# Optimization experiments

Hardware: AMD Instinct MI355X
Metric: run time of the kernel (lower is better)

The kernel has to match this reference:

```python
import jax, jax.numpy as jnp
import numpy as np

B, S, D_IN, H, L = 8, 4096, 256, 512, 2
EPS = 1e-5


def layer_norm(x, w, b):
    mu = x.mean(axis=-1, keepdims=True)
    var = ((x - mu) ** 2).mean(axis=-1, keepdims=True)
    return (x - mu) * jax.lax.rsqrt(var + EPS) * w + b


def rwkv_scan(k, v):
    # wkv_t = sigmoid(k_t)*v_t + alpha_{t-1};  alpha_t = sigmoid(k_t)*v_t + 0.9*alpha_{t-1}
    s = jax.nn.sigmoid(k) * v  # [B,S,H]
    def step(alpha, s_t):
        wkv_t = s_t + alpha
        return s_t + 0.9 * alpha, wkv_t
    _, wkv = jax.lax.scan(step, jnp.zeros_like(s[:, 0]), jnp.swapaxes(s, 0, 1))
    return jnp.swapaxes(wkv, 0, 1)


def setup_inputs() -> dict:
    key = jax.random.key(0)
    ks = jax.random.split(key, 16)
    sc = 1.0 / np.sqrt(H)
    return {
        "x": jax.random.normal(ks[0], (B, S, D_IN), jnp.float32),
        "W_in": jax.random.normal(ks[1], (H, D_IN), jnp.float32) / np.sqrt(D_IN),
        "b_in": jnp.zeros((H,), jnp.float32),
        "tm_k": jax.random.normal(ks[2], (L, H), jnp.float32),
        "tm_v": jax.random.normal(ks[3], (L, H), jnp.float32),
        "tm_r": jax.random.normal(ks[4], (L, H), jnp.float32),
        "Wk": jax.random.normal(ks[5], (L, H, H), jnp.float32) * sc,
        "Wv": jax.random.normal(ks[6], (L, H, H), jnp.float32) * sc,
        "Wr": jax.random.normal(ks[7], (L, H, H), jnp.float32) * sc,
        "Wo": jax.random.normal(ks[8], (L, H, H), jnp.float32) * sc,
        "ln1_w": jnp.ones((L, H), jnp.float32),
        "ln1_b": jnp.zeros((L, H), jnp.float32),
        "ln2_w": jnp.ones((L, H), jnp.float32),
        "ln2_b": jnp.zeros((L, H), jnp.float32),
    }


def reference(x, W_in, b_in, tm_k, tm_v, tm_r, Wk, Wv, Wr, Wo, ln1_w, ln1_b, ln2_w, ln2_b):
    h = jnp.einsum('bsd,hd->bsh', x, W_in) + b_in  # input projection
    for l in range(L):
        mean = h.mean(axis=1, keepdims=True)  # [B,1,H]
        xk = h * tm_k[l] + (1 - tm_k[l]) * mean
        xv = h * tm_v[l] + (1 - tm_v[l]) * mean
        xr = h * tm_r[l] + (1 - tm_r[l]) * mean
        k = jax.nn.relu(jnp.einsum('bsh,oh->bso', xk, Wk[l]))
        v = jax.nn.relu(jnp.einsum('bsh,oh->bso', xv, Wv[l]))
        r = jax.nn.sigmoid(jnp.einsum('bsh,oh->bso', xr, Wr[l]))
        wkv = rwkv_scan(k, v)
        out = jnp.einsum('bsh,oh->bso', r * wkv, Wo[l])
        out = layer_norm(h + out, ln1_w[l], ln1_b[l])
        ff = jax.nn.relu(layer_norm(out, ln2_w[l], ln2_b[l]))
        h = out + ff
    return h
```

## Files before the change

kernel.cpp:

```cpp
#include <hip/hip_runtime.h>
#include <hip/hip_bf16.h>
#include <cstdint>
#include <cstddef>

#define S_LEN 4096
#define HDIM  512
#define BDIM  8
#define DIN   256
#define NLAYER 2

using float4v = __attribute__((ext_vector_type(4))) float;
using short8  = __attribute__((ext_vector_type(8))) short;
using bf16x8  = __attribute__((ext_vector_type(8))) __bf16;

struct __align__(8) us4_t { unsigned short x, y, z, w; };

__device__ __forceinline__ unsigned short f2bf(float f) {
    return __builtin_bit_cast(unsigned short, (__bf16)f);
}
__device__ __forceinline__ float bf2f(unsigned short s) {
    union { unsigned u; float f; } v; v.u = ((unsigned)s) << 16;
    return v.f;
}
__device__ __forceinline__ float fast_rcp(float x) { return __builtin_amdgcn_rcpf(x); }
__device__ __forceinline__ float fast_rsq(float x) { return __builtin_amdgcn_rsqf(x); }

__device__ __forceinline__ float4v mfma_bf16(short8 a, short8 b, float4v c) {
    return __builtin_amdgcn_mfma_f32_16x16x32_bf16(
        __builtin_bit_cast(bf16x8, a), __builtin_bit_cast(bf16x8, b), c, 0, 0, 0);
}
__device__ __forceinline__ float wave_sum(float v) {
#pragma unroll
    for (int m = 1; m < 64; m <<= 1) v += __shfl_xor(v, m, 64);
    return v;
}
__device__ __forceinline__ void gload16(const void* g, void* l) {
    __builtin_amdgcn_global_load_lds(
        (const __attribute__((address_space(1))) unsigned int*)g,
        (__attribute__((address_space(3))) unsigned int*)l,
        16, 0, 0);
}

#define VMW_ASM(N) asm volatile("s_waitcnt vmcnt(" #N ")" ::: "memory")
template<int N> __device__ __forceinline__ void vmwait() {
    static_assert(N == 0 || N == 4 || N == 5 || N == 6 || N == 8 || N == 10,
                  "add a case for this N");
    if constexpr (N == 0) VMW_ASM(0);
    else if constexpr (N == 4) VMW_ASM(4);
    else if constexpr (N == 5) VMW_ASM(5);
    else if constexpr (N == 6) VMW_ASM(6);
    else if constexpr (N == 8) VMW_ASM(8);
    else if constexpr (N == 10) VMW_ASM(10);
}
#define LGKM0()    asm volatile("s_waitcnt lgkmcnt(0)" ::: "memory")
#define RBARRIER() asm volatile("s_barrier" ::: "memory")

__global__ void cvt4_k(const float* __restrict__ a, unsigned short* __restrict__ oa, int na4,
                       const float* __restrict__ b, unsigned short* __restrict__ ob, int nb4,
                       const float* __restrict__ c, unsigned short* __restrict__ oc2, int nc4,
                       const float* __restrict__ Wk, const float* __restrict__ Wv,
                       const float* __restrict__ Wr,
                       const float* __restrict__ tmk, const float* __restrict__ tmv,
                       const float* __restrict__ tmr,
                       unsigned short* __restrict__ Wf, int nf4)
{
    int i = blockIdx.x * blockDim.x + threadIdx.x;
    if (i < na4 + nb4 + nc4) {
        const float* src; unsigned short* dst; int idx;
        if (i < na4)            { src = a; dst = oa;  idx = i; }
        else if (i < na4 + nb4) { src = b; dst = ob;  idx = i - na4; }
        else                    { src = c; dst = oc2; idx = i - na4 - nb4; }
        float4 v = ((const float4*)src)[idx];
        us4_t o;
        o.x = f2bf(v.x); o.y = f2bf(v.y); o.z = f2bf(v.z); o.w = f2bf(v.w);
        ((us4_t*)dst)[idx] = o;
        return;
    }
    int fi = i - (na4 + nb4 + nc4);
    if (fi >= nf4) return;
    int e = fi * 4;
    const int HH = HDIM * HDIM;
    int l   = (e >= 3 * HH) ? 1 : 0;
    int rem = e - l * 3 * HH;
    int j   = rem >> 18;
    int ok  = rem & (HH - 1);
    int k   = ok & (HDIM - 1);
    const float* W = (j == 0) ? Wk : (j == 1) ? Wv : Wr;
    const float* t = (j == 0) ? tmk : (j == 1) ? tmv : tmr;
    float4 w = *(const float4*)(W + (size_t)l * HH + ok);
    const float* tp = t + l * HDIM + k;
    us4_t o;
    o.x = f2bf(w.x * tp[0]); o.y = f2bf(w.y * tp[1]);
    o.z = f2bf(w.z * tp[2]); o.w = f2bf(w.w * tp[3]);
    *(us4_t*)(Wf + e) = o;
}

__global__ void meanbias_k(const float* __restrict__ msum_l, float invS,
    const float* __restrict__ Wk, const float* __restrict__ Wv, const float* __restrict__ Wr,
    const float* __restrict__ tmk, const float* __restrict__ tmv, const float* __restrict__ tmr,
    float* __restrict__ mb)
{
    __shared__ float m2[HDIM];
    const int j = blockIdx.x, b = blockIdx.y, oc = blockIdx.z;
    const int tid = threadIdx.x, lane = tid & 63, wid = tid >> 6;
    const float* W = (j == 0) ? Wk : (j == 1) ? Wv : Wr;
    const float* t = (j == 0) ? tmk : (j == 1) ? tmv : tmr;
    for (int i = tid; i < HDIM; i += 256)
        m2[i] = msum_l[b * HDIM + i] * invS * (1.f - t[i]);
    __syncthreads();
    const int o0 = oc * 64 + wid * 16;
    for (int oo = 0; oo < 16; oo++) {
        int o = o0 + oo;
        const float* wr_ = W + (size_t)o * HDIM + lane * 8;
        float4 w0 = *(const float4*)wr_;
        float4 w1 = *(const float4*)(wr_ + 4);
        const float* mp = m2 + lane * 8;
        float s = w0.x * mp[0] + w0.y * mp[1] + w0.z * mp[2] + w0.w * mp[3]
                + w1.x * mp[4] + w1.y * mp[5] + w1.z * mp[6] + w1.w * mp[7];
        s = wave_sum(s);
        if (lane == 0) mb[((size_t)j * BDIM + b) * HDIM + o] = s;
    }
}

template<int TM, int BN, int NMAT, int EPI, int K, int NY, int NW>
__global__ __launch_bounds__(NW * 64, 2) void gemm2_k(
    const unsigned short* __restrict__ A,
    const unsigned short* __restrict__ B0,
    const unsigned short* __restrict__ B1,
    const unsigned short* __restrict__ B2,
    const float* __restrict__ mb,
    unsigned short* __restrict__ outB0,
    unsigned short* __restrict__ outB1,
    float* __restrict__ msum_out)
{
    constexpr int NTHR = NW * 64;
    constexpr int NT   = K / 64;
    static_assert(NT >= 2, "pipeline needs >=2 K-tiles");
    constexpr int ROWS = TM + NMAT * BN;
    constexpr int NC   = ROWS / 8;
    static_assert(NC % NW == 0, "chunks must split evenly across waves");
    constexpr int NCW  = NC / NW;
    constexpr int WC   = NW / 2;
    constexpr int MI   = TM / 32;
    constexpr int CW   = BN / WC;
    constexpr int NI   = CW / 16;
    static_assert(NI >= 1, "");
    __shared__ __align__(16) unsigned short smem[2][ROWS * 64];
    static_assert((EPI == 1 ? 2 : 1) * TM * (BN + 8) <= 2 * ROWS * 64,
                  "epilogue overflow");

    const int tid = threadIdx.x, lane = tid & 63, wid = tid >> 6;
    const int wr = wid / WC, wc = wid % WC;
    const int chunk = gridDim.x >> 3;
    const int logical = (blockIdx.x & 7) * chunk + (blockIdx.x >> 3);
    const int m0 = (logical / NY) * TM, n0 = (logical % NY) * BN;

    const int l8 = lane >> 3;
    const int soff = (((lane & 7) ^ l8) * 16);
    const char* gp[NCW];
#pragma unroll
    for (int i = 0; i < NCW; i++) {
        int c = wid * NCW + i;
        const unsigned short* base; int row;
        if (c < TM / 8) { base = A; row = m0 + c * 8 + l8; }
        else {
            int cb = c - TM / 8;
            int j  = cb / (BN / 8);
            int rl = (cb % (BN / 8)) * 8 + l8;
            base = (j == 0) ? B0 : ((j == 1) ? B1 : B2);
            row  = n0 + rl;
        }
        gp[i] = (const char*)base + (size_t)row * (K * 2) + soff;
    }

    float4v acc[NMAT][MI][NI];
#pragma unroll
    for (int j = 0; j < NMAT; j++)
#pragma unroll
        for (int mi = 0; mi < MI; mi++)
#pragma unroll
            for (int ni = 0; ni < NI; ni++)
                acc[j][mi][ni] = (float4v){0.f, 0.f, 0.f, 0.f};

    auto STAGE = [&](int buf) {
#pragma unroll
        for (int i = 0; i < NCW; i++) {
            gload16(gp[i], (char*)&smem[buf][0] + (unsigned)(wid * NCW + i) * 1024);
            gp[i] += 128;
        }
    };

    STAGE(0);
    STAGE(1);
    for (int t = 0; t < NT; t++) {
        if (t == NT - 1) vmwait<0>(); else vmwait<NCW>();
        RBARRIER();
        const int cur = t & 1;
        const unsigned short* As = &smem[cur][0];
        const unsigned short* Bs = &smem[cur][TM * 64];
#pragma unroll
        for (int kk = 0; kk < 2; kk++) {
            short8 a_[MI];
#pragma unroll
            for (int mi = 0; mi < MI; mi++) {
                int row = wr * (TM / 2) + mi * 16 + (lane & 15);
                int sl  = (kk * 4 + (lane >> 4)) ^ (row & 7);
                a_[mi] = *(const short8*)&As[row * 64 + sl * 8];
            }
#pragma unroll
            for (int ni = 0; ni < NI; ni++) {
                int rowb = wc * CW + ni * 16 + (lane & 15);
                int slb  = (kk * 4 + (lane >> 4)) ^ (rowb & 7);
#pragma unroll
                for (int j = 0; j < NMAT; j++) {
                    short8 b_ = *(const short8*)&Bs[(j * BN + rowb) * 64 + slb * 8];
#pragma unroll
                    for (int mi = 0; mi < MI; mi++)
                        acc[j][mi][ni] = mfma_bf16(a_[mi], b_, acc[j][mi][ni]);
                }
            }
        }
        LGKM0();
        RBARRIER();
        if (t + 2 < NT) STAGE(cur);
    }

    const int bidx  = m0 >> 12;
    const int rbl   = wr * (TM / 2) + (lane >> 4) * 4;
    const int cbl   = wc * CW + (lane & 15);

    if constexpr (EPI == 0) {
        constexpr int BNP = BN + 8;
        unsigned short* tile = &smem[0][0];
        float csum[NI];
#pragma unroll
        for (int ni = 0; ni < NI; ni++) csum[ni] = 0.f;
#pragma unroll
        for (int ni = 0; ni < NI; ni++) {
            float bb = mb[n0 + cbl + ni * 16];
#pragma unroll
            for (int mi = 0; mi < MI; mi++) {
#pragma unroll
                for (int r = 0; r < 4; r++) {
                    float val = acc[0][mi][ni][r] + bb;
                    tile[(rbl + mi * 16 + r) * BNP + cbl + ni * 16] = f2bf(val);
                    csum[ni] += val;
                }
            }
        }
        __syncthreads();
        constexpr int QR = BN / 8;
        for (int idx = tid; idx < TM * QR; idx += NTHR) {
            int row = idx / QR, q = idx % QR;
            int4 v = *(const int4*)&tile[row * BNP + q * 8];
            *(int4*)(outB0 + (size_t)(m0 + row) * HDIM + n0 + q * 8) = v;
        }
#pragma unroll
        for (int ni = 0; ni < NI; ni++) {
            float sc = csum[ni];
            sc += __shfl_xor(sc, 16, 64);
            sc += __shfl_xor(sc, 32, 64);
            if (lane < 16)
                atomicAdd(&msum_out[bidx * HDIM + n0 + wc * CW + ni * 16 + lane], sc);
        }
    } else if constexpr (EPI == 1) {
        constexpr int BNP = BN + 8;
        unsigned short* tS = &smem[0][0];
        unsigned short* tR = &smem[0][0] + TM * BNP;
#pragma unroll
        for (int ni = 0; ni < NI; ni++) {
            int gcol = n0 + cbl + ni * 16;
            float mk = mb[(0 * BDIM + bidx) * HDIM + gcol];
            float mv = mb[(1 * BDIM + bidx) * HDIM + gcol];
            float mr = mb[(2 * BDIM + bidx) * HDIM + gcol];
#pragma unroll
            for (int mi = 0; mi < MI; mi++) {
#pragma unroll
                for (int r = 0; r < 4; r++) {
                    float kk_ = fmaxf(acc[0][mi][ni][r] + mk, 0.f);
                    float vv  = fmaxf(acc[NMAT > 1 ? 1 : 0][mi][ni][r] + mv, 0.f);
                    float rr  = fast_rcp(1.f + __expf(-(acc[NMAT > 2 ? 2 : 0][mi][ni][r] + mr)));
                    float sv  = vv * fast_rcp(1.f + __expf(-kk_));
                    int loc = (rbl + mi * 16 + r) * BNP + cbl + ni * 16;
                    tS[loc] = f2bf(sv);
                    tR[loc] = f2bf(rr);
                }
            }
        }
        __syncthreads();
        constexpr int QR = BN / 8;
        for (int idx = tid; idx < 2 * TM * QR; idx += NTHR) {
            int tn = idx / (TM * QR), rem = idx % (TM * QR);
            int row = rem / QR, q = rem % QR;
            int4 v = *(const int4*)&smem[0][tn * TM * BNP + row * BNP + q * 8];
            unsigned short* dst = tn ? outB1 : outB0;
            *(int4*)(dst + (size_t)(m0 + row) * HDIM + n0 + q * 8) = v;
        }
    } else {
        constexpr int BNP = BN + 8;
        unsigned short* tile = &smem[0][0];
#pragma unroll
        for (int ni = 0; ni < NI; ni++) {
#pragma unroll
            for (int mi = 0; mi < MI; mi++) {
#pragma unroll
                for (int r = 0; r < 4; r++)
                    tile[(rbl + mi * 16 + r) * BNP + cbl + ni * 16] = f2bf(acc[0][mi][ni][r]);
            }
        }
        __syncthreads();
        constexpr int QR = BN / 8;
        for (int idx = tid; idx < TM * QR; idx += NTHR) {
            int row = idx / QR, q = idx % QR;
            int4 v = *(const int4*)&tile[row * BNP + q * 8];
            *(int4*)(outB0 + (size_t)(m0 + row) * HDIM + n0 + q * 8) = v;
        }
    }
}

__global__ void scan_k(const unsigned short* __restrict__ s_bf,
                       const unsigned short* __restrict__ r_bf,
                       unsigned short* __restrict__ y_bf)
{
    const int C = 64, W = 64;
    const int b  = blockIdx.z;
    const int t0 = blockIdx.x * C;
    const int h2 = threadIdx.x * 2;
    const size_t rowbase = (size_t)b * S_LEN;

    float a0 = 0.f, a1 = 0.f;
    int tstart = t0 - W; if (tstart < 0) tstart = 0;
#pragma unroll 4
    for (int t = tstart; t < t0; t++) {
        unsigned u = *(const unsigned*)(s_bf + (rowbase + t) * HDIM + h2);
        a0 = bf2f((unsigned short)(u & 0xffff)) + 0.9f * a0;
        a1 = bf2f((unsigned short)(u >> 16))    + 0.9f * a1;
    }
#pragma unroll 4
    for (int t = t0; t < t0 + C; t++) {
        size_t off = (rowbase + t) * HDIM + h2;
        unsigned u  = *(const unsigned*)(s_bf + off);
        unsigned ur = *(const unsigned*)(r_bf + off);
        float s0 = bf2f((unsigned short)(u & 0xffff));
        float s1 = bf2f((unsigned short)(u >> 16));
        float w0 = s0 + a0, w1v = s1 + a1;
        a0 = s0 + 0.9f * a0;
        a1 = s1 + 0.9f * a1;
        float r0 = bf2f((unsigned short)(ur & 0xffff));
        float r1 = bf2f((unsigned short)(ur >> 16));
        unsigned outp = (unsigned)f2bf(r0 * w0) | ((unsigned)f2bf(r1 * w1v) << 16);
        *(unsigned*)(y_bf + off) = outp;
    }
}

__global__ __launch_bounds__(256) void lnfuse_k(
    const unsigned short* __restrict__ Hb, const unsigned short* __restrict__ O,
    const float* __restrict__ w1, const float* __restrict__ b1,
    const float* __restrict__ w2, const float* __restrict__ b2,
    float* __restrict__ dstF, unsigned short* __restrict__ dst_bf,
    float* __restrict__ msum_next)
{
    __shared__ float red[HDIM];
    const int b    = blockIdx.y;
    const int tid  = threadIdx.x;
    const int wid  = tid >> 6, lane = tid & 63;
    const int wglob = blockIdx.x * 4 + wid;
    const int c0   = lane * 8;

    float w1v[8], b1v[8], w2v[8], b2v[8];
#pragma unroll
    for (int j = 0; j < 8; j++) {
        w1v[j] = w1[c0 + j]; b1v[j] = b1[c0 + j];
        w2v[j] = w2[c0 + j]; b2v[j] = b2[c0 + j];
    }
    float macc[8] = {0.f, 0.f, 0.f, 0.f, 0.f, 0.f, 0.f, 0.f};

    for (int s = wglob; s < S_LEN; s += 512) {
        size_t ro = ((size_t)b * S_LEN + s) * HDIM + c0;
        int4 hv4 = *(const int4*)(Hb + ro);
        int4 ov4 = *(const int4*)(O + ro);
        const unsigned short* hu = (const unsigned short*)&hv4;
        const unsigned short* ou = (const unsigned short*)&ov4;
        float x[8];
#pragma unroll
        for (int j = 0; j < 8; j++) x[j] = bf2f(hu[j]) + bf2f(ou[j]);
        float sm = 0.f;
#pragma unroll
        for (int j = 0; j < 8; j++) sm += x[j];
        float mu = wave_sum(sm) * (1.f / HDIM);
        float sq = 0.f;
#pragma unroll
        for (int j = 0; j < 8; j++) { float d = x[j] - mu; sq += d * d; }
        float rs = fast_rsq(wave_sum(sq) * (1.f / HDIM) + 1e-5f);
        float out[8];
#pragma unroll
        for (int j = 0; j < 8; j++) out[j] = (x[j] - mu) * rs * w1v[j] + b1v[j];
        float sm2 = 0.f;
#pragma unroll
        for (int j = 0; j < 8; j++) sm2 += out[j];
        float mu2 = wave_sum(sm2) * (1.f / HDIM);
        float sq2 = 0.f;
#pragma unroll
        for (int j = 0; j < 8; j++) { float d = out[j] - mu2; sq2 += d * d; }
        float rs2 = fast_rsq(wave_sum(sq2) * (1.f / HDIM) + 1e-5f);
        float hn[8];
#pragma unroll
        for (int j = 0; j < 8; j++) {
            float ff = fmaxf(0.f, (out[j] - mu2) * rs2 * w2v[j] + b2v[j]);
            hn[j] = out[j] + ff;
            macc[j] += hn[j];
        }
        if (dstF) {
            float4 o1 = {hn[0], hn[1], hn[2], hn[3]};
            float4 o2 = {hn[4], hn[5], hn[6], hn[7]};
            *(float4*)(dstF + ro) = o1;
            *(float4*)(dstF + ro + 4) = o2;
        }
        if (dst_bf) {
            unsigned q[4];
#pragma unroll
            for (int j = 0; j < 4; j++)
                q[j] = (unsigned)f2bf(hn[2 * j]) | ((unsigned)f2bf(hn[2 * j + 1]) << 16);
            *(int4*)(dst_bf + ro) = *(int4*)q;
        }
    }

    if (msum_next) {
        for (int i = tid; i < HDIM; i += 256) red[i] = 0.f;
        __syncthreads();
#pragma unroll
        for (int j = 0; j < 8; j++) atomicAdd(&red[c0 + j], macc[j]);
        __syncthreads();
        for (int i = tid; i < HDIM; i += 256)
            atomicAdd(&msum_next[b * HDIM + i], red[i]);
    }
}

extern "C" void kernel_launch(void* const* d_in, const int* in_sizes, int n_in,
                              void* d_out, int out_size, void* d_ws, size_t ws_size,
                              hipStream_t stream)
{
    const float* x   = (const float*)d_in[0];
    const float* Win = (const float*)d_in[1];
    const float* bin = (const float*)d_in[2];
    const float* tmk = (const float*)d_in[3];
    const float* tmv = (const float*)d_in[4];
    const float* tmr = (const float*)d_in[5];
    const float* Wk  = (const float*)d_in[6];
    const float* Wv  = (const float*)d_in[7];
    const float* Wr  = (const float*)d_in[8];
    const float* Wo  = (const float*)d_in[9];
    const float* l1w = (const float*)d_in[10];
    const float* l1b = (const float*)d_in[11];
    const float* l2w = (const float*)d_in[12];
    const float* l2b = (const float*)d_in[13];

    char* ws = (char*)d_ws;
    size_t off = 0;
    auto alloc = [&](size_t bytes) -> char* {
        char* p = ws + off;
        off += (bytes + 255) & ~(size_t)255;
        return p;
    };
    const size_t NTOK = (size_t)BDIM * S_LEN;
    const size_t HH = (size_t)HDIM * HDIM;
    unsigned short* region0 = (unsigned short*)alloc(NTOK * HDIM * 2);
    unsigned short* x_bf   = region0;
    unsigned short* y_bf   = region0;
    unsigned short* Win_bf = (unsigned short*)alloc((size_t)HDIM * DIN * 2);
    unsigned short* Wo_bf  = (unsigned short*)alloc(NLAYER * HH * 2);
    unsigned short* Wf     = (unsigned short*)alloc(NLAYER * 3 * HH * 2);
    unsigned short* h_bf   = (unsigned short*)alloc(NTOK * HDIM * 2);
    unsigned short* h2_bf  = (unsigned short*)alloc(NTOK * HDIM * 2);
    unsigned short* s_bf   = (unsigned short*)alloc(NTOK * HDIM * 2);
    unsigned short* r_bf   = (unsigned short*)alloc(NTOK * HDIM * 2);
    unsigned short* o_bf   = (unsigned short*)alloc(NTOK * HDIM * 2);
    float*          msum   = (float*)alloc(2 * BDIM * HDIM * 4);
    float*          mbuf   = (float*)alloc(3 * BDIM * HDIM * 4);

    hipMemsetAsync(msum, 0, 2 * BDIM * HDIM * 4, stream);

    {
        int na4 = (int)(NTOK * DIN / 4);
        int nb4 = (int)((size_t)HDIM * DIN / 4);
        int nc4 = (int)(NLAYER * HH / 4);
        int nf4 = (int)(NLAYER * 3 * HH / 4);
        int tot = na4 + nb4 + nc4 + nf4;
        cvt4_k<<<(tot + 255) / 256, 256, 0, stream>>>(
            x, x_bf, na4, Win, Win_bf, nb4, Wo, Wo_bf, nc4,
            Wk, Wv, Wr, tmk, tmv, tmr, Wf, nf4);
    }

    const float invS = 1.f / S_LEN;

    gemm2_k<128, 128, 1, 0, DIN, 4, 4><<<1024, 256, 0, stream>>>(
        x_bf, Win_bf, nullptr, nullptr, bin, h_bf, nullptr, msum);

    for (int l = 0; l < NLAYER; l++) {
        const unsigned short* hl = (l == 0) ? h_bf : h2_bf;
        meanbias_k<<<dim3(3, BDIM, 8), 256, 0, stream>>>(
            msum + (size_t)l * BDIM * HDIM, invS,
            Wk + (size_t)l * HH, Wv + (size_t)l * HH, Wr + (size_t)l * HH,
            tmk + l * HDIM, tmv + l * HDIM, tmr + l * HDIM, mbuf);
        gemm2_k<128, 64, 3, 1, HDIM, 8, 8><<<2048, 512, 0, stream>>>(
            hl,
            Wf + ((size_t)l * 3 + 0) * HH, Wf + ((size_t)l * 3 + 1) * HH,
            Wf + ((size_t)l * 3 + 2) * HH,
            mbuf, s_bf, r_bf, nullptr);
        scan_k<<<dim3(S_LEN / 64, 1, BDIM), 256, 0, stream>>>(s_bf, r_bf, y_bf);
        gemm2_k<128, 128, 1, 3, HDIM, 4, 4><<<1024, 256, 0, stream>>>(
            y_bf, Wo_bf + (size_t)l * HH, nullptr, nullptr,
            nullptr, o_bf, nullptr, nullptr);
        lnfuse_k<<<dim3(128, BDIM), 256, 0, stream>>>(
            hl, o_bf, l1w + l * HDIM, l1b + l * HDIM, l2w + l * HDIM, l2b + l * HDIM,
            (l == 0) ? nullptr : (float*)d_out,
            (l == 0) ? h2_bf : nullptr,
            (l == 0) ? (msum + BDIM * HDIM) : nullptr);
    }
}
```

Baseline: 316.2 us.

## Fuse output projection GEMM with residual double layernorm epilogue

Replaces the separate Wo GEMM plus lnfuse kernel with one GEMM that uses full-row tiles (TM=64, BN=512), so each block owns complete rows and can run residual add, both layernorms, ReLU and the mean-sum accumulation in its epilogue. This removes the o_bf intermediate write and re-read and one kernel launch. In exchange the GEMM grid shrinks to 512 blocks with larger tiles, which may lower occupancy and change how well the tiling performs.

```diff
diff --git a/kernel.cpp b/kernel.cpp
--- a/kernel.cpp
+++ b/kernel.cpp
@@ -43,13 +43,14 @@
 
 #define VMW_ASM(N) asm volatile("s_waitcnt vmcnt(" #N ")" ::: "memory")
 template<int N> __device__ __forceinline__ void vmwait() {
-    static_assert(N == 0 || N == 4 || N == 5 || N == 6 || N == 8 || N == 10,
+    static_assert(N == 0 || N == 4 || N == 5 || N == 6 || N == 8 || N == 9 || N == 10,
                   "add a case for this N");
     if constexpr (N == 0) VMW_ASM(0);
     else if constexpr (N == 4) VMW_ASM(4);
     else if constexpr (N == 5) VMW_ASM(5);
     else if constexpr (N == 6) VMW_ASM(6);
     else if constexpr (N == 8) VMW_ASM(8);
+    else if constexpr (N == 9) VMW_ASM(9);
     else if constexpr (N == 10) VMW_ASM(10);
 }
 #define LGKM0()    asm volatile("s_waitcnt lgkmcnt(0)" ::: "memory")
@@ -129,8 +130,12 @@
     const unsigned short* __restrict__ B1,
     const unsigned short* __restrict__ B2,
     const float* __restrict__ mb,
+    const float* __restrict__ mb2,
+    const float* __restrict__ mb3,
+    const float* __restrict__ mb4,
     unsigned short* __restrict__ outB0,
     unsigned short* __restrict__ outB1,
+    float* __restrict__ dstF,
     float* __restrict__ msum_out)
 {
     constexpr int NTHR = NW * 64;
@@ -146,7 +151,8 @@
     constexpr int NI   = CW / 16;
     static_assert(NI >= 1, "");
     __shared__ __align__(16) unsigned short smem[2][ROWS * 64];
-    static_assert((EPI == 1 ? 2 : 1) * TM * (BN + 8) <= 2 * ROWS * 64,
+    static_assert((EPI == 4 ? TM * (BN + 12) * 2
+                            : (EPI == 1 ? 2 : 1) * TM * (BN + 8)) <= 2 * ROWS * 64,
                   "epilogue overflow");
 
     const int tid = threadIdx.x, lane = tid & 63, wid = tid >> 6;
@@ -295,6 +301,92 @@
             int4 v = *(const int4*)&smem[0][tn * TM * BNP + row * BNP + q * 8];
             unsigned short* dst = tn ? outB1 : outB0;
             *(int4*)(dst + (size_t)(m0 + row) * HDIM + n0 + q * 8) = v;
+        }
+    } else if constexpr (EPI == 4) {
+        constexpr int BNP4 = BN + 12;
+        float* ftile = (float*)&smem[0][0];
+#pragma unroll
+        for (int ni = 0; ni < NI; ni++)
+#pragma unroll
+            for (int mi = 0; mi < MI; mi++)
+#pragma unroll
+                for (int r = 0; r < 4; r++)
+                    ftile[(rbl + mi * 16 + r) * BNP4 + cbl + ni * 16] = acc[0][mi][ni][r];
+        __syncthreads();
+        const int c0 = lane * 8;
+        float w1v[8], b1v[8], w2v[8], b2v[8];
+#pragma unroll
+        for (int j = 0; j < 8; j++) {
+            w1v[j] = mb[c0 + j];  b1v[j] = mb2[c0 + j];
+            w2v[j] = mb3[c0 + j]; b2v[j] = mb4[c0 + j];
+        }
+        constexpr int RPW = TM / NW;
+        float macc[8] = {0.f, 0.f, 0.f, 0.f, 0.f, 0.f, 0.f, 0.f};
+        int4 hv[RPW];
+#pragma unroll
+        for (int rr = 0; rr < RPW; rr++) {
+            int row = wid * RPW + rr;
+            hv[rr] = *(const int4*)(B1 + (size_t)(m0 + row) * HDIM + c0);
+        }
+#pragma unroll
+        for (int rr = 0; rr < RPW; rr++) {
+            int row = wid * RPW + rr;
+            const unsigned short* hu = (const unsigned short*)&hv[rr];
+            const float* op = &ftile[row * BNP4 + c0];
+            float x[8];
+#pragma unroll
+            for (int j = 0; j < 8; j++) x[j] = bf2f(hu[j]) + op[j];
+            float sm = 0.f;
+#pragma unroll
+            for (int j = 0; j < 8; j++) sm += x[j];
+            float mu = wave_sum(sm) * (1.f / HDIM);
+            float sq = 0.f;
+#pragma unroll
+            for (int j = 0; j < 8; j++) { float d = x[j] - mu; sq += d * d; }
+            float rs = fast_rsq(wave_sum(sq) * (1.f / HDIM) + 1e-5f);
+            float out[8];
+#pragma unroll
+            for (int j = 0; j < 8; j++) out[j] = (x[j] - mu) * rs * w1v[j] + b1v[j];
+            float sm2 = 0.f;
+#pragma unroll
+            for (int j = 0; j < 8; j++) sm2 += out[j];
+            float mu2 = wave_sum(sm2) * (1.f / HDIM);
+            float sq2 = 0.f;
+#pragma unroll
+            for (int j = 0; j < 8; j++) { float d = out[j] - mu2; sq2 += d * d; }
+            float rs2 = fast_rsq(wave_sum(sq2) * (1.f / HDIM) + 1e-5f);
+            float hn[8];
+#pragma unroll
+            for (int j = 0; j < 8; j++) {
+                float ff = fmaxf(0.f, (out[j] - mu2) * rs2 * w2v[j] + b2v[j]);
+                hn[j] = out[j] + ff;
+                macc[j] += hn[j];
+            }
+            size_t ro = (size_t)(m0 + row) * HDIM + c0;
+            if (dstF) {
+                float4 o1 = {hn[0], hn[1], hn[2], hn[3]};
+                float4 o2 = {hn[4], hn[5], hn[6], hn[7]};
+                *(float4*)(dstF + ro) = o1;
+                *(float4*)(dstF + ro + 4) = o2;
+            }
+            if (outB0) {
+                unsigned q[4];
+#pragma unroll
+                for (int j = 0; j < 4; j++)
+                    q[j] = (unsigned)f2bf(hn[2 * j]) | ((unsigned)f2bf(hn[2 * j + 1]) << 16);
+                *(int4*)(outB0 + ro) = *(int4*)q;
+            }
+        }
+        if (msum_out) {
+            __syncthreads();
+            float* red = ftile;
+            if (tid < HDIM) red[tid] = 0.f;
+            __syncthreads();
+#pragma unroll
+            for (int j = 0; j < 8; j++) atomicAdd(&red[c0 + j], macc[j]);
+            __syncthreads();
+            if (tid < HDIM)
+                atomicAdd(&msum_out[bidx * HDIM + tid], red[tid]);
         }
     } else {
         constexpr int BNP = BN + 8;
@@ -350,89 +442,6 @@
         float r1 = bf2f((unsigned short)(ur >> 16));
         unsigned outp = (unsigned)f2bf(r0 * w0) | ((unsigned)f2bf(r1 * w1v) << 16);
         *(unsigned*)(y_bf + off) = outp;
-    }
-}
-
-__global__ __launch_bounds__(256) void lnfuse_k(
-    const unsigned short* __restrict__ Hb, const unsigned short* __restrict__ O,
-    const float* __restrict__ w1, const float* __restrict__ b1,
-    const float* __restrict__ w2, const float* __restrict__ b2,
-    float* __restrict__ dstF, unsigned short* __restrict__ dst_bf,
-    float* __restrict__ msum_next)
-{
-    __shared__ float red[HDIM];
-    const int b    = blockIdx.y;
-    const int tid  = threadIdx.x;
-    const int wid  = tid >> 6, lane = tid & 63;
-    const int wglob = blockIdx.x * 4 + wid;
-    const int c0   = lane * 8;
-
-    float w1v[8], b1v[8], w2v[8], b2v[8];
-#pragma unroll
-    for (int j = 0; j < 8; j++) {
-        w1v[j] = w1[c0 + j]; b1v[j] = b1[c0 + j];
-        w2v[j] = w2[c0 + j]; b2v[j] = b2[c0 + j];
-    }
-    float macc[8] = {0.f, 0.f, 0.f, 0.f, 0.f, 0.f, 0.f, 0.f};
-
-    for (int s = wglob; s < S_LEN; s += 512) {
-        size_t ro = ((size_t)b * S_LEN + s) * HDIM + c0;
-        int4 hv4 = *(const int4*)(Hb + ro);
-        int4 ov4 = *(const int4*)(O + ro);
-        const unsigned short* hu = (const unsigned short*)&hv4;
-        const unsigned short* ou = (const unsigned short*)&ov4;
-        float x[8];
-#pragma unroll
-        for (int j = 0; j < 8; j++) x[j] = bf2f(hu[j]) + bf2f(ou[j]);
-        float sm = 0.f;
-#pragma unroll
-        for (int j = 0; j < 8; j++) sm += x[j];
-        float mu = wave_sum(sm) * (1.f / HDIM);
-        float sq = 0.f;
-#pragma unroll
-        for (int j = 0; j < 8; j++) { float d = x[j] - mu; sq += d * d; }
-        float rs = fast_rsq(wave_sum(sq) * (1.f / HDIM) + 1e-5f);
-        float out[8];
-#pragma unroll
-        for (int j = 0; j < 8; j++) out[j] = (x[j] - mu) * rs * w1v[j] + b1v[j];
-        float sm2 = 0.f;
-#pragma unroll
-        for (int j = 0; j < 8; j++) sm2 += out[j];
-        float mu2 = wave_sum(sm2) * (1.f / HDIM);
-        float sq2 = 0.f;
-#pragma unroll
-        for (int j = 0; j < 8; j++) { float d = out[j] - mu2; sq2 += d * d; }
-        float rs2 = fast_rsq(wave_sum(sq2) * (1.f / HDIM) + 1e-5f);
-        float hn[8];
-#pragma unroll
-        for (int j = 0; j < 8; j++) {
-            float ff = fmaxf(0.f, (out[j] - mu2) * rs2 * w2v[j] + b2v[j]);
-            hn[j] = out[j] + ff;
-            macc[j] += hn[j];
-        }
-        if (dstF) {
-            float4 o1 = {hn[0], hn[1], hn[2], hn[3]};
-            float4 o2 = {hn[4], hn[5], hn[6], hn[7]};
-            *(float4*)(dstF + ro) = o1;
-            *(float4*)(dstF + ro + 4) = o2;
-        }
-        if (dst_bf) {
-            unsigned q[4];
-#pragma unroll
-            for (int j = 0; j < 4; j++)
-                q[j] = (unsigned)f2bf(hn[2 * j]) | ((unsigned)f2bf(hn[2 * j + 1]) << 16);
-            *(int4*)(dst_bf + ro) = *(int4*)q;
-        }
-    }
-
-    if (msum_next) {
-        for (int i = tid; i < HDIM; i += 256) red[i] = 0.f;
-        __syncthreads();
-#pragma unroll
-        for (int j = 0; j < 8; j++) atomicAdd(&red[c0 + j], macc[j]);
-        __syncthreads();
-        for (int i = tid; i < HDIM; i += 256)
-            atomicAdd(&msum_next[b * HDIM + i], red[i]);
     }
 }
 
@@ -474,7 +483,6 @@
     unsigned short* h2_bf  = (unsigned short*)alloc(NTOK * HDIM * 2);
     unsigned short* s_bf   = (unsigned short*)alloc(NTOK * HDIM * 2);
     unsigned short* r_bf   = (unsigned short*)alloc(NTOK * HDIM * 2);
-    unsigned short* o_bf   = (unsigned short*)alloc(NTOK * HDIM * 2);
     float*          msum   = (float*)alloc(2 * BDIM * HDIM * 4);
     float*          mbuf   = (float*)alloc(3 * BDIM * HDIM * 4);
 
@@ -494,7 +502,8 @@
     const float invS = 1.f / S_LEN;
 
     gemm2_k<128, 128, 1, 0, DIN, 4, 4><<<1024, 256, 0, stream>>>(
-        x_bf, Win_bf, nullptr, nullptr, bin, h_bf, nullptr, msum);
+        x_bf, Win_bf, nullptr, nullptr, bin, nullptr, nullptr, nullptr,
+        h_bf, nullptr, nullptr, msum);
 
     for (int l = 0; l < NLAYER; l++) {
         const unsigned short* hl = (l == 0) ? h_bf : h2_bf;
@@ -506,15 +515,13 @@
             hl,
             Wf + ((size_t)l * 3 + 0) * HH, Wf + ((size_t)l * 3 + 1) * HH,
             Wf + ((size_t)l * 3 + 2) * HH,
-            mbuf, s_bf, r_bf, nullptr);
+            mbuf, nullptr, nullptr, nullptr, s_bf, r_bf, nullptr, nullptr);
         scan_k<<<dim3(S_LEN / 64, 1, BDIM), 256, 0, stream>>>(s_bf, r_bf, y_bf);
-        gemm2_k<128, 128, 1, 3, HDIM, 4, 4><<<1024, 256, 0, stream>>>(
-            y_bf, Wo_bf + (size_t)l * HH, nullptr, nullptr,
-            nullptr, o_bf, nullptr, nullptr);
-        lnfuse_k<<<dim3(128, BDIM), 256, 0, stream>>>(
-            hl, o_bf, l1w + l * HDIM, l1b + l * HDIM, l2w + l * HDIM, l2b + l * HDIM,
+        gemm2_k<64, 512, 1, 4, HDIM, 1, 8><<<512, 512, 0, stream>>>(
+            y_bf, Wo_bf + (size_t)l * HH, hl, nullptr,
+            l1w + l * HDIM, l1b + l * HDIM, l2w + l * HDIM, l2b + l * HDIM,
+            (l == 0) ? h2_bf : nullptr, nullptr,
             (l == 0) ? nullptr : (float*)d_out,
-            (l == 0) ? h2_bf : nullptr,
             (l == 0) ? (msum + BDIM * HDIM) : nullptr);
     }
 }
```

Result: no change. 317.8 us (+0.5%).
